# Kernel tuning notes

Measured on AMD Instinct MI355X. Metric: run time of the kernel, lower is better.

Reference implementation:

```python
import jax, jax.numpy as jnp
import numpy as np


def _lstm_layer(xs, W_ih, W_hh, b):
    # xs: [T, B, D]; W_ih: [4H, D]; W_hh: [4H, H]; b: [4H] (b_ih + b_hh)
    T, B, _ = xs.shape
    H = W_hh.shape[1]
    # precompute input projection for all timesteps: [T, B, 4H]
    x_proj = jnp.einsum('tbd,gd->tbg', xs, W_ih) + b

    def step(carry, xp):
        h, c = carry
        gates = xp + h @ W_hh.T                      # [B, 4H]
        i, f, g, o = jnp.split(gates, 4, axis=-1)    # torch gate order i,f,g,o
        i = jax.nn.sigmoid(i)
        f = jax.nn.sigmoid(f)
        g = jnp.tanh(g)
        o = jax.nn.sigmoid(o)
        c = f * c + i * g
        h = o * jnp.tanh(c)
        return (h, c), h

    h0 = jnp.zeros((B, H), xs.dtype)
    c0 = jnp.zeros((B, H), xs.dtype)
    (h_T, c_T), outs = jax.lax.scan(step, (h0, c0), x_proj)
    return outs, h_T, c_T  # outs: [T, B, H]


def setup_inputs() -> dict:
    key = jax.random.key(0)
    ks = jax.random.split(key, 8)
    B, T, D, H, C = 64, 256, 512, 1024, 1000
    s = 0.05
    return {
        'x': jax.random.normal(ks[0], (B, T, D), jnp.float32),
        'W_ih0': jax.random.normal(ks[1], (4 * H, D), jnp.float32) * s,
        'W_hh0': jax.random.normal(ks[2], (4 * H, H), jnp.float32) * s,
        'b_ih0': jnp.zeros((4 * H,), jnp.float32),
        'b_hh0': jnp.zeros((4 * H,), jnp.float32),
        'W_ih1': jax.random.normal(ks[3], (4 * H, H), jnp.float32) * s,
        'W_hh1': jax.random.normal(ks[4], (4 * H, H), jnp.float32) * s,
        'b_ih1': jnp.zeros((4 * H,), jnp.float32),
        'b_hh1': jnp.zeros((4 * H,), jnp.float32),
        'W_fc': jax.random.normal(ks[5], (C, 2 * H), jnp.float32) * s,
        'b_fc': jnp.zeros((C,), jnp.float32),
    }


def reference(x, W_ih0, W_hh0, b_ih0, b_hh0, W_ih1, W_hh1, b_ih1, b_hh1, W_fc, b_fc):
    # x: [B, T, D] -> time-major [T, B, D]
    xs = jnp.swapaxes(x, 0, 1)
    outs0, h0_T, _ = _lstm_layer(xs, W_ih0, W_hh0, b_ih0 + b_hh0)
    # inter-layer dropout is identity at inference
    outs1, h1_T, _ = _lstm_layer(outs0, W_ih1, W_hh1, b_ih1 + b_hh1)
    # concat final hidden states of all layers: [B, 2H]
    h_final = jnp.concatenate([h0_T, h1_T], axis=-1)
    logits = h_final @ W_fc.T + b_fc  # [B, C]
    return logits
```

## Files before the change

### kernel.cpp

```cpp
#include <hip/hip_runtime.h>

#define BB 64
#define TT 256
#define DD 512
#define HH 1024
#define NCLS 1000

#define NB   256
#define L0B  128
#define COLS 8
#define RING 64
#define HSZ  (BB * HH)
#define CHK0 48
#define CHK1 64
#define TS0  (CHK0 * 512)
#define TS1  (CHK1 * 512)
#define GRP  32
#define EPSLP 4
#define DYNLDS (2 * TS1 * 2 + 4 * 64 * 8 * 4 + 64 * 8 * 2)
#define BARWORDS ((2 * L0B + 2 * GRP) * 32)

typedef _Float16 f16;
typedef _Float16 f16x4 __attribute__((ext_vector_type(4)));
typedef _Float16 f16x8 __attribute__((ext_vector_type(8)));
typedef float f32x4 __attribute__((ext_vector_type(4)));
typedef int i32x4 __attribute__((ext_vector_type(4)));

#define MFMA16(af, bf, acc) __builtin_amdgcn_mfma_f32_16x16x32_f16((af), (bf), (acc), 0, 0, 0)
#define FSIG(x) (1.f / (1.f + __expf(-(x))))
#define FTANH(x) (1.f - 2.f / (__expf(2.f * (x)) + 1.f))
#define ALOAD __HIP_MEMORY_SCOPE_AGENT

template <int N, int I = 0>
__device__ __forceinline__ void glP(i32x4* A, const f16* base) {
  if constexpr (I < N) {
    asm volatile("global_load_dwordx4 %0, %1, off offset:%2"
                 : "=v"(A[I]) : "v"(base + (I >> 2) * 2048), "n"((I & 3) * 1024));
    glP<N, I + 1>(A, base);
  }
}
template <int TOTAL, int EXTRA, int BBASE, int G = 0>
__device__ __forceinline__ void mf2(i32x4* A, const f16* w0, const f16* w1,
                                    f32x4& a0, f32x4& a1, f32x4& b0, f32x4& b1) {
  if constexpr (G * 8 < TOTAL) {
    asm volatile("s_waitcnt vmcnt(%0)" :: "n"(TOTAL - (G + 1) * 8 + EXTRA)
                 : "memory");
    __builtin_amdgcn_sched_barrier(0);
    #pragma unroll
    for (int k = 0; k < 8; ++k) {
      int ck = G * 8 + k;
      f16x8 a;
      __builtin_memcpy(&a, &A[ck], 16);
      const f16* p0 = w0 + (size_t)(BBASE + ck) * 512;
      const f16* p1 = w1 + (size_t)(BBASE + ck) * 512;
      if (ck & 1) {
        a1 = MFMA16(a, *(const f16x8*)p0, a1);
        b1 = MFMA16(a, *(const f16x8*)p1, b1);
      } else {
        a0 = MFMA16(a, *(const f16x8*)p0, a0);
        b0 = MFMA16(a, *(const f16x8*)p1, b0);
      }
    }
    mf2<TOTAL, EXTRA, BBASE, G + 1>(A, w0, w1, a0, a1, b0, b1);
  }
}

__global__ __launch_bounds__(256) void prep_x_kernel(const float* __restrict__ x,
                                                     f16* __restrict__ xpk) {
  int idx = blockIdx.x * 256 + threadIdx.x;
  int seg = idx & 63;
  int b   = (idx >> 6) & 63;
  int t   = idx >> 12;
  float4 u = *(const float4*)(x + ((size_t)b * TT + t) * DD + seg * 8);
  float4 v = *(const float4*)(x + ((size_t)b * TT + t) * DD + seg * 8 + 4);
  f16x8 o = {(f16)u.x, (f16)u.y, (f16)u.z, (f16)u.w,
             (f16)v.x, (f16)v.y, (f16)v.z, (f16)v.w};
  int ch = seg >> 2, kgrp = seg & 3;
  *(f16x8*)(xpk + ((size_t)((t * 4 + (b >> 4)) * 16 + ch) * 64 +
                   kgrp * 16 + (b & 15)) * 8) = o;
}

__global__ __launch_bounds__(512, 2) void lstm_persistent(
    const f16* __restrict__ xpk,
    const float* __restrict__ Wih0, const float* __restrict__ Whh0,
    const float* __restrict__ bih0, const float* __restrict__ bhh0,
    const float* __restrict__ Wih1, const float* __restrict__ Whh1,
    const float* __restrict__ bih1, const float* __restrict__ bhh1,
    f16* __restrict__ h0ring, f16* __restrict__ h1ring, int* __restrict__ bar) {
  extern __shared__ f16 lds[];
  const int bid  = blockIdx.x;
  const bool IS1 = (bid >= L0B);
  const int j0   = (IS1 ? bid - L0B : bid) * COLS;
  const int tid  = threadIdx.x;
  const int wv   = tid >> 6;
  const int lane = tid & 63;
  const int kh   = wv >> 2;
  const int bt   = wv & 3;
  const int col  = lane & 15;
  const int kgrp = lane >> 4;
  const int jc   = col & 7;
  const int ch0  = j0 >> 5;
  const int kg0  = (j0 >> 3) & 3;

  const int CHK = IS1 ? CHK1 : CHK0;
  const int TS  = IS1 ? TS1 : TS0;
  const int DIN = IS1 ? HH : DD;
  f16* Wpk    = lds;
  float* pbuf = (float*)(lds + 2 * TS1);
  f16* hbuf   = (f16*)(pbuf + 4 * 64 * 8);

  {
    const float* Wi = IS1 ? Wih1 : Wih0;
    const float* Wh = IS1 ? Whh1 : Whh0;
    const int grow = (kh * 2 + (col >> 3)) * HH + j0 + jc;
    const float* rowi = Wi + (size_t)grow * DIN;
    const float* rowh = Wh + (size_t)grow * HH;
    for (int ck = bt; ck < CHK; ck += 4) {
      int k = ck * 32 + kgrp * 8;
      const float* src = (k < DIN) ? (rowi + k) : (rowh + (k - DIN));
      float4 u = *(const float4*)src;
      float4 v = *(const float4*)(src + 4);
      f16x8 w = {(f16)u.x, (f16)u.y, (f16)u.z, (f16)u.w,
                 (f16)v.x, (f16)v.y, (f16)v.z, (f16)v.w};
      *(f16x8*)(Wpk + (size_t)kh * TS + (size_t)ck * 512 + lane * 8) = w;
    }
  }
  const float* bi = IS1 ? bih1 : bih0;
  const float* bh = IS1 ? bhh1 : bhh0;
  const int g0 = (col < 8) ? 0 : 1;
  const int g1 = (col < 8) ? 2 : 3;
  const float bias0 = bi[g0 * HH + j0 + jc] + bh[g0 * HH + j0 + jc];
  const float bias1 = bi[g1 * HH + j0 + jc] + bh[g1 * HH + j0 + jc];
  __syncthreads();

  float creg[4] = {0.f, 0.f, 0.f, 0.f};
  int* flag0 = bar;
  int* flag1 = bar + L0B * 32;
  int* ep0   = bar + 2 * L0B * 32;
  int* ep1   = ep0 + GRP * 32;
  const int myrep = (IS1 ? bid - L0B : bid) & (GRP - 1);
  const f16* w0 = Wpk + lane * 8;
  const f16* w1 = Wpk + (size_t)TS + lane * 8;

  auto cellstore = [&](f32x4 aA0, f32x4 aA1, f32x4 aB0, f32x4 aB1, f16* hw) {
    if (kh == 1) {
      #pragma unroll
      for (int r = 0; r < 4; ++r) {
        pbuf[((size_t)bt * 64 + lane) * 8 + r]     = aA0[r] + aA1[r];
        pbuf[((size_t)bt * 64 + lane) * 8 + 4 + r] = aB0[r] + aB1[r];
      }
    }
    __syncthreads();
    if (kh == 0) {
      #pragma unroll
      for (int r = 0; r < 4; ++r) {
        float pv0 = aA0[r] + aA1[r] + pbuf[((size_t)bt * 64 + lane) * 8 + r] + bias0;
        float pv1 = aB0[r] + aB1[r] + pbuf[((size_t)bt * 64 + lane) * 8 + 4 + r] + bias1;
        float q0 = __shfl_xor(pv0, 8);
        float q1 = __shfl_xor(pv1, 8);
        if (col < 8) {
          float ig = FSIG(pv0);
          float fg = FSIG(q0);
          float gg = FTANH(pv1);
          float og = FSIG(q1);
          float cc = fg * creg[r] + ig * gg;
          creg[r] = cc;
          hbuf[((size_t)bt * 16 + kgrp * 4 + r) * 8 + jc] = (f16)(og * FTANH(cc));
        }
      }
      if (lane < 16) {
        f16x8 hv = *(const f16x8*)(hbuf + ((size_t)bt * 16 + lane) * 8);
        f16* dst = hw + ((size_t)(bt * 32 + ch0) * 64 + kg0 * 16 + lane) * 8;
        i32x4 hvi;
        __builtin_memcpy(&hvi, &hv, 16);
        asm volatile("global_store_dwordx4 %0, %1, off sc1"
                     :: "v"(dst), "v"(hvi) : "memory");
      }
    }
  };

  if (!IS1) {
    const bool AGG = (bid == 0);
    i32x4 af[16];
    for (int t = 0; t < TT; ++t) {
      f32x4 aA0 = {0.f,0.f,0.f,0.f}, aA1 = {0.f,0.f,0.f,0.f};
      f32x4 aB0 = {0.f,0.f,0.f,0.f}, aB1 = {0.f,0.f,0.f,0.f};
      if (kh == 0) {
        const f16* ax = xpk + (size_t)(t * 4 + bt) * 16 * 512 + lane * 8;
        glP<16>(af, ax);
        mf2<16, 0, 0>(af, w0, w1, aA0, aA1, aB0, aB1);
      }
      if (AGG) {
        if (tid < L0B)
          while (__hip_atomic_load(flag0 + tid * 32, __ATOMIC_RELAXED, ALOAD) < t)
            __builtin_amdgcn_s_sleep(1);
      } else if (tid == 0) {
        while (__hip_atomic_load(ep0 + myrep * 32, __ATOMIC_RELAXED, ALOAD) < t)
          __builtin_amdgcn_s_sleep(EPSLP);
      }
      if (tid == 256) {
        while (__hip_atomic_load(ep1 + myrep * 32, __ATOMIC_RELAXED, ALOAD) < t - (RING - 1))
          __builtin_amdgcn_s_sleep(EPSLP);
      }
      __syncthreads();
      if (AGG && tid < GRP)
        __hip_atomic_store(ep0 + tid * 32, t, __ATOMIC_RELAXED, ALOAD);
      const f16* hp = h0ring + (size_t)((t - 1) & (RING - 1)) * HSZ +
                      (size_t)(bt * 32 + kh * 16) * 512 + lane * 8;
      glP<16>(af, hp);
      if (kh == 0) mf2<16, 0, 16>(af, w0, w1, aA0, aA1, aB0, aB1);
      else         mf2<16, 0, 32>(af, w0, w1, aA0, aA1, aB0, aB1);
      cellstore(aA0, aA1, aB0, aB1,
                h0ring + (size_t)(t & (RING - 1)) * HSZ);
      asm volatile("s_waitcnt vmcnt(0)" ::: "memory");
      __syncthreads();
      if (tid == 0)
        __hip_atomic_store(flag0 + bid * 32, t + 1, __ATOMIC_RELAXED, ALOAD);
    }
    if (AGG) {
      if (tid < L0B)
        while (__hip_atomic_load(flag0 + tid * 32, __ATOMIC_RELAXED, ALOAD) < TT)
          __builtin_amdgcn_s_sleep(1);
      __syncthreads();
      if (tid < GRP)
        __hip_atomic_store(ep0 + tid * 32, TT, __ATOMIC_RELAXED, ALOAD);
    }
  } else {
    const bool AGG = (bid == L0B);
    i32x4 af[32];
    for (int u = 0; u < TT; ++u) {
      if (AGG) {
        if (tid < L0B)
          while (__hip_atomic_load(flag1 + tid * 32, __ATOMIC_RELAXED, ALOAD) < u)
            __builtin_amdgcn_s_sleep(1);
        if (tid == 256)
          while (__hip_atomic_load(ep0 + myrep * 32, __ATOMIC_RELAXED, ALOAD) < u + 1)
            __builtin_amdgcn_s_sleep(EPSLP);
        __syncthreads();
        if (tid < GRP)
          __hip_atomic_store(ep1 + tid * 32, u, __ATOMIC_RELAXED, ALOAD);
      } else {
        if (tid == 0)
          while (__hip_atomic_load(ep0 + myrep * 32, __ATOMIC_RELAXED, ALOAD) < u + 1)
            __builtin_amdgcn_s_sleep(EPSLP);
        __syncthreads();
      }
      f32x4 aA0 = {0.f,0.f,0.f,0.f}, aA1 = {0.f,0.f,0.f,0.f};
      f32x4 aB0 = {0.f,0.f,0.f,0.f}, aB1 = {0.f,0.f,0.f,0.f};
      if (kh == 0) {
        const f16* h0p = h0ring + (size_t)(u & (RING - 1)) * HSZ +
                         (size_t)bt * 32 * 512 + lane * 8;
        glP<32>(af, h0p);
        mf2<32, 0, 0>(af, w0, w1, aA0, aA1, aB0, aB1);
      }
      if (!AGG) {
        if (tid == 0)
          while (__hip_atomic_load(ep1 + myrep * 32, __ATOMIC_RELAXED, ALOAD) < u)
            __builtin_amdgcn_s_sleep(EPSLP);
        __syncthreads();
      }
      if (kh == 1) {
        const f16* h1p = h1ring + (size_t)((u - 1) & (RING - 1)) * HSZ +
                         (size_t)bt * 32 * 512 + lane * 8;
        glP<32>(af, h1p);
        mf2<32, 0, 32>(af, w0, w1, aA0, aA1, aB0, aB1);
      }
      cellstore(aA0, aA1, aB0, aB1,
                h1ring + (size_t)(u & (RING - 1)) * HSZ);
      asm volatile("s_waitcnt vmcnt(0)" ::: "memory");
      __syncthreads();
      if (tid == 0)
        __hip_atomic_store(flag1 + (bid - L0B) * 32, u + 1, __ATOMIC_RELAXED, ALOAD);
    }
  }
}

__global__ __launch_bounds__(256) void fc_kernel(const f16* __restrict__ h0f,
                                                 const f16* __restrict__ h1f,
                                                 const float* __restrict__ Wfc,
                                                 const float* __restrict__ bfc,
                                                 float* __restrict__ out) {
  __shared__ f16 hl[64][264];
  __shared__ float Wl[4][260];
  const int tid = threadIdx.x;
  const int cl0 = blockIdx.x * 4;
  const int b   = tid >> 2;
  const int cq  = tid & 3;
  float a = 0.f;
  for (int k0 = 0; k0 < 2 * HH; k0 += 256) {
    #pragma unroll
    for (int i = 0; i < 8; i++) {
      int v   = tid + i * 256;
      int row = v >> 5;
      int kk  = (v & 31) * 8;
      int kg  = k0 + kk;
      int kg2 = (kg < HH) ? kg : kg - HH;
      const f16* bse = (kg < HH) ? h0f : h1f;
      const f16* src = bse + ((size_t)((row >> 4) * 32 + (kg2 >> 5)) * 64 +
                              ((kg2 >> 3) & 3) * 16 + (row & 15)) * 8;
      *(f16x8*)(&hl[row][kk]) = *(const f16x8*)src;
    }
    {
      int row = tid >> 6;
      int kk  = (tid & 63) * 4;
      *(float4*)(&Wl[row][kk]) = *(const float4*)(Wfc + (size_t)(cl0 + row) * (2 * HH) + k0 + kk);
    }
    __syncthreads();
    #pragma unroll 8
    for (int k = 0; k < 256; k++) a += (float)hl[b][k] * Wl[cq][k];
    __syncthreads();
  }
  out[(size_t)b * NCLS + cl0 + cq] = a + bfc[cl0 + cq];
}

extern "C" void kernel_launch(void* const* d_in, const int* in_sizes, int n_in,
                              void* d_out, int out_size, void* d_ws, size_t ws_size,
                              hipStream_t stream) {
  const float* x    = (const float*)d_in[0];
  const float* Wih0 = (const float*)d_in[1];
  const float* Whh0 = (const float*)d_in[2];
  const float* bih0 = (const float*)d_in[3];
  const float* bhh0 = (const float*)d_in[4];
  const float* Wih1 = (const float*)d_in[5];
  const float* Whh1 = (const float*)d_in[6];
  const float* bih1 = (const float*)d_in[7];
  const float* bhh1 = (const float*)d_in[8];
  const float* Wfc  = (const float*)d_in[9];
  const float* bfc  = (const float*)d_in[10];
  float* out = (float*)d_out;

  char* p = (char*)d_ws;
  auto alloc = [&](size_t bytes) {
    char* r = p;
    p += (bytes + 255) & ~(size_t)255;
    return r;
  };
  f16* xpk    = (f16*)alloc((size_t)BB * TT * DD * 2);
  f16* h0ring = (f16*)alloc((size_t)RING * HSZ * 2);
  f16* h1ring = (f16*)alloc((size_t)RING * HSZ * 2);
  int* bar    = (int*)alloc((size_t)BARWORDS * 4);

  if ((size_t)(p - (char*)d_ws) > ws_size) return;

  (void)hipMemsetAsync(bar, 0, (size_t)BARWORDS * 4, stream);
  (void)hipMemsetAsync(h0ring + (size_t)(RING - 1) * HSZ, 0, (size_t)HSZ * 2, stream);
  (void)hipMemsetAsync(h1ring + (size_t)(RING - 1) * HSZ, 0, (size_t)HSZ * 2, stream);

  prep_x_kernel<<<dim3(TT * BB * (DD / 8) / 256), dim3(256), 0, stream>>>(x, xpk);

  (void)hipFuncSetAttribute((const void*)lstm_persistent,
                            hipFuncAttributeMaxDynamicSharedMemorySize, DYNLDS);
  lstm_persistent<<<dim3(NB), dim3(512), DYNLDS, stream>>>(
      xpk, Wih0, Whh0, bih0, bhh0, Wih1, Whh1, bih1, bhh1, h0ring, h1ring, bar);

  fc_kernel<<<dim3(NCLS / 4), dim3(256), 0, stream>>>(
      h0ring + (size_t)(RING - 1) * HSZ, h1ring + (size_t)(RING - 1) * HSZ,
      Wfc, bfc, out);
}
```

Baseline: 1.613 ms.

## Prefetch next-step input operands and rebalance K-halves in persistent LSTM kernel

Layer-0 blocks now load the next timestep's x-projection operands into registers right after publishing the current step. Layer-1 blocks likewise prefetch the next h0 slice after the step, moving the layer-0 dependency wait to the end of the iteration. Layer 1 also splits its recurrent h1 operand across both K-halves, so each wave does part of the recurrent GEMM instead of one half doing all of it. The LDS partial-sum buffer stride is padded from 8 to 9 floats to reduce bank conflicts. The extra live register arrays raise VGPR pressure, and the reordered waits change the synchronisation structure.

```diff
diff --git a/kernel.cpp b/kernel.cpp
--- a/kernel.cpp
+++ b/kernel.cpp
@@ -17,7 +17,7 @@
 #define TS1  (CHK1 * 512)
 #define GRP  32
 #define EPSLP 4
-#define DYNLDS (2 * TS1 * 2 + 4 * 64 * 8 * 4 + 64 * 8 * 2)
+#define DYNLDS (2 * TS1 * 2 + 4 * 64 * 9 * 4 + 64 * 8 * 2)
 #define BARWORDS ((2 * L0B + 2 * GRP) * 32)
 
 typedef _Float16 f16;
@@ -107,7 +107,7 @@
   const int DIN = IS1 ? HH : DD;
   f16* Wpk    = lds;
   float* pbuf = (float*)(lds + 2 * TS1);
-  f16* hbuf   = (f16*)(pbuf + 4 * 64 * 8);
+  f16* hbuf   = (f16*)(pbuf + 4 * 64 * 9);
 
   {
     const float* Wi = IS1 ? Wih1 : Wih0;
@@ -146,16 +146,16 @@
     if (kh == 1) {
       #pragma unroll
       for (int r = 0; r < 4; ++r) {
-        pbuf[((size_t)bt * 64 + lane) * 8 + r]     = aA0[r] + aA1[r];
-        pbuf[((size_t)bt * 64 + lane) * 8 + 4 + r] = aB0[r] + aB1[r];
+        pbuf[((size_t)bt * 64 + lane) * 9 + r]     = aA0[r] + aA1[r];
+        pbuf[((size_t)bt * 64 + lane) * 9 + 4 + r] = aB0[r] + aB1[r];
       }
     }
     __syncthreads();
     if (kh == 0) {
       #pragma unroll
       for (int r = 0; r < 4; ++r) {
-        float pv0 = aA0[r] + aA1[r] + pbuf[((size_t)bt * 64 + lane) * 8 + r] + bias0;
-        float pv1 = aB0[r] + aB1[r] + pbuf[((size_t)bt * 64 + lane) * 8 + 4 + r] + bias1;
+        float pv0 = aA0[r] + aA1[r] + pbuf[((size_t)bt * 64 + lane) * 9 + r] + bias0;
+        float pv1 = aB0[r] + aB1[r] + pbuf[((size_t)bt * 64 + lane) * 9 + 4 + r] + bias1;
         float q0 = __shfl_xor(pv0, 8);
         float q1 = __shfl_xor(pv1, 8);
         if (col < 8) {
@@ -181,15 +181,11 @@
 
   if (!IS1) {
     const bool AGG = (bid == 0);
-    i32x4 af[16];
+    i32x4 afs[16];
+    i32x4 afc[16];
+    if (kh == 0)
+      glP<16>(afs, xpk + (size_t)(0 * 4 + bt) * 16 * 512 + lane * 8);
     for (int t = 0; t < TT; ++t) {
-      f32x4 aA0 = {0.f,0.f,0.f,0.f}, aA1 = {0.f,0.f,0.f,0.f};
-      f32x4 aB0 = {0.f,0.f,0.f,0.f}, aB1 = {0.f,0.f,0.f,0.f};
-      if (kh == 0) {
-        const f16* ax = xpk + (size_t)(t * 4 + bt) * 16 * 512 + lane * 8;
-        glP<16>(af, ax);
-        mf2<16, 0, 0>(af, w0, w1, aA0, aA1, aB0, aB1);
-      }
       if (AGG) {
         if (tid < L0B)
           while (__hip_atomic_load(flag0 + tid * 32, __ATOMIC_RELAXED, ALOAD) < t)
@@ -207,15 +203,23 @@
         __hip_atomic_store(ep0 + tid * 32, t, __ATOMIC_RELAXED, ALOAD);
       const f16* hp = h0ring + (size_t)((t - 1) & (RING - 1)) * HSZ +
                       (size_t)(bt * 32 + kh * 16) * 512 + lane * 8;
-      glP<16>(af, hp);
-      if (kh == 0) mf2<16, 0, 16>(af, w0, w1, aA0, aA1, aB0, aB1);
-      else         mf2<16, 0, 32>(af, w0, w1, aA0, aA1, aB0, aB1);
-      cellstore(aA0, aA1, aB0, aB1,
-                h0ring + (size_t)(t & (RING - 1)) * HSZ);
+      f32x4 aA0 = {0.f,0.f,0.f,0.f}, aA1 = {0.f,0.f,0.f,0.f};
+      f32x4 aB0 = {0.f,0.f,0.f,0.f}, aB1 = {0.f,0.f,0.f,0.f};
+      if (kh == 0) {
+        glP<16>(afc, hp);
+        mf2<16, 16, 0>(afs, w0, w1, aA0, aA1, aB0, aB1);
+        mf2<16, 0, 16>(afc, w0, w1, aA0, aA1, aB0, aB1);
+      } else {
+        glP<16>(afc, hp);
+        mf2<16, 0, 32>(afc, w0, w1, aA0, aA1, aB0, aB1);
+      }
+      cellstore(aA0, aA1, aB0, aB1, h0ring + (size_t)(t & (RING - 1)) * HSZ);
       asm volatile("s_waitcnt vmcnt(0)" ::: "memory");
       __syncthreads();
       if (tid == 0)
         __hip_atomic_store(flag0 + bid * 32, t + 1, __ATOMIC_RELAXED, ALOAD);
+      if (kh == 0 && t + 1 < TT)
+        glP<16>(afs, xpk + (size_t)((t + 1) * 4 + bt) * 16 * 512 + lane * 8);
     }
     if (AGG) {
       if (tid < L0B)
@@ -227,50 +231,56 @@
     }
   } else {
     const bool AGG = (bid == L0B);
-    i32x4 af[32];
+    i32x4 afs[32];
+    i32x4 afc[16];
+    {
+      if (tid == 0)
+        while (__hip_atomic_load(ep0 + myrep * 32, __ATOMIC_RELAXED, ALOAD) < 1)
+          __builtin_amdgcn_s_sleep(EPSLP);
+      __syncthreads();
+      if (kh == 0)
+        glP<32>(afs, h0ring + (size_t)0 * HSZ + (size_t)bt * 32 * 512 + lane * 8);
+    }
     for (int u = 0; u < TT; ++u) {
       if (AGG) {
         if (tid < L0B)
           while (__hip_atomic_load(flag1 + tid * 32, __ATOMIC_RELAXED, ALOAD) < u)
             __builtin_amdgcn_s_sleep(1);
-        if (tid == 256)
-          while (__hip_atomic_load(ep0 + myrep * 32, __ATOMIC_RELAXED, ALOAD) < u + 1)
-            __builtin_amdgcn_s_sleep(EPSLP);
         __syncthreads();
         if (tid < GRP)
           __hip_atomic_store(ep1 + tid * 32, u, __ATOMIC_RELAXED, ALOAD);
       } else {
         if (tid == 0)
-          while (__hip_atomic_load(ep0 + myrep * 32, __ATOMIC_RELAXED, ALOAD) < u + 1)
+          while (__hip_atomic_load(ep1 + myrep * 32, __ATOMIC_RELAXED, ALOAD) < u)
             __builtin_amdgcn_s_sleep(EPSLP);
         __syncthreads();
       }
+      const f16* h1p = h1ring + (size_t)((u - 1) & (RING - 1)) * HSZ +
+                       (size_t)(bt * 32 + kh * 16) * 512 + lane * 8;
       f32x4 aA0 = {0.f,0.f,0.f,0.f}, aA1 = {0.f,0.f,0.f,0.f};
       f32x4 aB0 = {0.f,0.f,0.f,0.f}, aB1 = {0.f,0.f,0.f,0.f};
       if (kh == 0) {
-        const f16* h0p = h0ring + (size_t)(u & (RING - 1)) * HSZ +
-                         (size_t)bt * 32 * 512 + lane * 8;
-        glP<32>(af, h0p);
-        mf2<32, 0, 0>(af, w0, w1, aA0, aA1, aB0, aB1);
-      }
-      if (!AGG) {
-        if (tid == 0)
-          while (__hip_atomic_load(ep1 + myrep * 32, __ATOMIC_RELAXED, ALOAD) < u)
+        glP<16>(afc, h1p);
+        mf2<32, 16, 0>(afs, w0, w1, aA0, aA1, aB0, aB1);
+        mf2<16, 0, 32>(afc, w0, w1, aA0, aA1, aB0, aB1);
+      } else {
+        glP<16>(afc, h1p);
+        mf2<16, 0, 48>(afc, w0, w1, aA0, aA1, aB0, aB1);
+      }
+      cellstore(aA0, aA1, aB0, aB1, h1ring + (size_t)(u & (RING - 1)) * HSZ);
+      asm volatile("s_waitcnt vmcnt(0)" ::: "memory");
+      __syncthreads();
+      if (tid == 0)
+        __hip_atomic_store(flag1 + (bid - L0B) * 32, u + 1, __ATOMIC_RELAXED, ALOAD);
+      if (u + 1 < TT) {
+        if (tid == 256)
+          while (__hip_atomic_load(ep0 + myrep * 32, __ATOMIC_RELAXED, ALOAD) < u + 2)
             __builtin_amdgcn_s_sleep(EPSLP);
         __syncthreads();
-      }
-      if (kh == 1) {
-        const f16* h1p = h1ring + (size_t)((u - 1) & (RING - 1)) * HSZ +
-                         (size_t)bt * 32 * 512 + lane * 8;
-        glP<32>(af, h1p);
-        mf2<32, 0, 32>(af, w0, w1, aA0, aA1, aB0, aB1);
-      }
-      cellstore(aA0, aA1, aB0, aB1,
-                h1ring + (size_t)(u & (RING - 1)) * HSZ);
-      asm volatile("s_waitcnt vmcnt(0)" ::: "memory");
-      __syncthreads();
-      if (tid == 0)
-        __hip_atomic_store(flag1 + (bid - L0B) * 32, u + 1, __ATOMIC_RELAXED, ALOAD);
+        if (kh == 0)
+          glP<32>(afs, h0ring + (size_t)((u + 1) & (RING - 1)) * HSZ +
+                       (size_t)bt * 32 * 512 + lane * 8);
+      }
     }
   }
 }
```

Result: faster. 1.350 ms (-16.3%).
